# Kernel optimization log

Hardware: AMD Instinct MI355X
Metric: run time of the kernel (lower is better)

## Reference

```python
import jax, jax.numpy as jnp
from jax import lax
import numpy as np

KERNEL_SIZE = 29
N_T = 1000
SIGMA_MIN, SIGMA_MAX = 0.5, 20.0
HIDDEN = 32


def _gaussian_kernel1d(sigma, ksize):
    # torchvision: linspace over [-half, half], normalized gaussian pdf
    half = (ksize - 1) * 0.5
    xg = jnp.linspace(-half, half, ksize)
    pdf = jnp.exp(-0.5 * (xg / sigma) ** 2)
    return pdf / pdf.sum()


def batch_blur(x, sigmas, ksize=KERNEL_SIZE):
    # x: [B,C,H,W], sigmas: [B]. Per-sample separable gaussian blur as a single
    # grouped depthwise conv (feature_group_count = B*C) instead of a Python loop.
    B, C, H, W = x.shape
    k1 = jax.vmap(lambda s: _gaussian_kernel1d(s, ksize))(sigmas)  # [B, k]
    pad = ksize // 2
    xp = jnp.pad(x, ((0, 0), (0, 0), (pad, pad), (pad, pad)), mode='reflect')
    lhs = xp.reshape(1, B * C, H + 2 * pad, W + 2 * pad)
    kbc = jnp.repeat(k1, C, axis=0)  # [B*C, k] per-channel kernel
    # vertical pass then horizontal pass (outer-product 2D kernel == two 1D passes)
    y = lax.conv_general_dilated(lhs, kbc[:, None, :, None], (1, 1), 'VALID',
                                 feature_group_count=B * C)
    y = lax.conv_general_dilated(y, kbc[:, None, None, :], (1, 1), 'VALID',
                                 feature_group_count=B * C)
    return y.reshape(B, C, H, W)


def gt_net(z, tn, W1, b1, tw, W2, b2):
    # simple time-conditioned conv net standing in for the opaque `gt` module
    h = lax.conv_general_dilated(z, W1, (1, 1), 'SAME')  # [B,HIDDEN,H,W]
    h = h + b1[None, :, None, None] + (tn[:, None] * tw[None, :])[:, :, None, None]
    h = jax.nn.relu(h)
    out = lax.conv_general_dilated(h, W2, (1, 1), 'SAME') + b2[None, :, None, None]
    return out


def setup_inputs() -> dict:
    key = jax.random.key(0)
    ks = jax.random.split(key, 6)
    B, C, H, W = 32, 3, 256, 256
    x = jax.random.normal(ks[0], (B, C, H, W), dtype=jnp.float32)
    t = jax.random.randint(ks[1], (B,), 0, N_T, dtype=jnp.int32)
    W1 = jax.random.normal(ks[2], (HIDDEN, C, 3, 3), dtype=jnp.float32) * 0.1
    b1 = jnp.zeros((HIDDEN,), dtype=jnp.float32)
    tw = jax.random.normal(ks[3], (HIDDEN,), dtype=jnp.float32) * 0.1
    W2 = jax.random.normal(ks[4], (C, HIDDEN, 3, 3), dtype=jnp.float32) * 0.1
    b2 = jnp.zeros((C,), dtype=jnp.float32)
    sigma_schedule = jnp.linspace(SIGMA_MIN, SIGMA_MAX, N_T, dtype=jnp.float32)
    return {"x": x, "t": t, "W1": W1, "b1": b1, "tw": tw, "W2": W2, "b2": b2,
            "sigma_schedule": sigma_schedule}


def reference(x, t, W1, b1, tw, W2, b2, sigma_schedule):
    sigma_t = sigma_schedule[t]                      # [B]
    z_t = batch_blur(x, sigma_t, KERNEL_SIZE)        # [B,C,H,W]
    preds = gt_net(z_t, t.astype(jnp.float32) / N_T, W1, b1, tw, W2, b2)
    return jnp.mean((x - preds) ** 2)                # MSELoss
```

## Files before the change

kernel.cpp:

```cpp
#include <hip/hip_runtime.h>
#include <hip/hip_bf16.h>

#define BATCH 32
#define CH 3
#define HH 256
#define WW 256
#define KS 29
#define PAD 14
#define NT_F 1000.0f

typedef __attribute__((ext_vector_type(8))) short short8;
typedef __attribute__((ext_vector_type(4))) float f32x4;
typedef __attribute__((ext_vector_type(16))) float f32x16;

union U4 { short8 s8; uint4 u4; };

__device__ inline unsigned short bf16rne(float f) {
  unsigned u = __float_as_uint(f);
  unsigned r = (u + 0x7FFFu + ((u >> 16) & 1u)) >> 16;
  return (unsigned short)r;
}
__device__ inline unsigned pk_bf16(float a, float b) {
  union { __hip_bfloat162 h2; unsigned u; } cv;
  cv.h2 = __float22bfloat162_rn(make_float2(a, b));
  return cv.u;
}


#define PARTIAL_OFF 3151872

__global__ __launch_bounds__(256, 3) void blur_kernel(
    const float* __restrict__ x, const int* __restrict__ t,
    const float* __restrict__ sched, const float* __restrict__ W1,
    const float* __restrict__ b1, const float* __restrict__ tw,
    const float* __restrict__ W2, float* __restrict__ ws,
    unsigned short* __restrict__ z) {
  int blk = blockIdx.x;
  int tid = threadIdx.x;

  if (blk >= BATCH * CH * 8) {
    float* tcond = ws + 1024;
    unsigned short* w1n = (unsigned short*)(ws + 2048);
    unsigned short* w2c = (unsigned short*)(ws + 2816);
    for (int i = tid; i < 1536; i += 256) {
      int mf = i >> 9, r = i & 511;
      int och = r >> 4, s = r & 15;
      int tp = mf * 4 + (s >> 2), ci = s & 3;
      w1n[i] = (ci < 3 && tp < 9) ? bf16rne(W1[och * 27 + ci * 9 + tp])
                                  : (unsigned short)0;
    }
    for (int i = tid; i < 4608; i += 256) {
      int tap = i >> 9, r = i & 511;
      int n = r >> 5, s = r & 31;
      int och = (s & 3) + 8 * ((s >> 2) & 3) + 4 * (s >> 4);
      int dy = tap / 3, dx = tap - dy * 3;
      w2c[i] = (n < 3) ? bf16rne(W2[((n * 32 + och) * 3 + dy) * 3 + dx])
                       : (unsigned short)0;
    }
    for (int i = tid; i < 1024; i += 256) {
      int b = i >> 5, o = i & 31;
      tcond[i] = b1[o] + ((float)t[b] * (1.0f / NT_F)) * tw[o];
    }
    return;
  }

  {
    int wid = (blk & 7) * 96 + (blk >> 3);
    blk = wid;
  }

  __shared__ float vsp[32][288];
  __shared__ float gkl[32];
  int rg = blk & 7;
  int bc = blk >> 3;
  int b = bc / CH;
  int y0 = rg * 32;
  const float* xp = x + (size_t)bc * (HH * WW);

  float xv[60];
#pragma unroll
  for (int i = 0; i < 60; i++) {
    int gy = y0 - PAD + i;
    gy = (gy < 0) ? -gy : gy;
    gy = (gy >= HH) ? (2 * HH - 2 - gy) : gy;
    xv[i] = xp[gy * WW + tid];
  }

  if (tid < 64) {
    float wexp = 0.0f;
    if (tid < KS) {
      float sigma = sched[t[b]];
      float xg = (float)(tid - PAD) / sigma;
      wexp = expf(-0.5f * xg * xg);
    }
    float s = wexp;
#pragma unroll
    for (int off = 32; off > 0; off >>= 1) s += __shfl_down(s, off);
    float tot = __shfl(s, 0);
    if (tid < 32) gkl[tid] = wexp / tot;
  }
  __syncthreads();

  float acc[32];
#pragma unroll
  for (int yy = 0; yy < 32; yy++) acc[yy] = 0.0f;
#pragma unroll
  for (int kk = 0; kk < KS; kk++) {
    float kv = gkl[kk];
#pragma unroll
    for (int yy = 0; yy < 32; yy++) acc[yy] += kv * xv[yy + kk];
  }
#pragma unroll
  for (int yy = 0; yy < 32; yy++) vsp[yy][tid + 16] = acc[yy];
  __syncthreads();
  {
    int row = tid >> 4, i2 = tid & 15;
#pragma unroll
    for (int r2 = 0; r2 < 2; r2++) {
      int rr = row + 16 * r2;
      vsp[rr][i2] = vsp[rr][32 - i2];
      vsp[rr][272 + i2] = vsp[rr][270 - i2];
    }
  }
  __syncthreads();

  size_t zb = (size_t)bc * (HH * WW);
#pragma unroll
  for (int it = 0; it < 8; ++it) {
    int unit = tid + 256 * it;
    int row = unit >> 6, cg = unit & 63;
    float w[36];
#pragma unroll
    for (int i = 0; i < 9; i++)
      *(float4*)&w[4 * i] = *(const float4*)&vsp[row][4 * (cg + i)];
    float o0 = 0, o1 = 0, o2 = 0, o3 = 0;
#pragma unroll
    for (int kk = 0; kk < KS; kk++) {
      float kv = gkl[kk];
      o0 += kv * w[2 + kk];
      o1 += kv * w[3 + kk];
      o2 += kv * w[4 + kk];
      o3 += kv * w[5 + kk];
    }
    unsigned u0 = pk_bf16(o0, o1);
    unsigned u1 = pk_bf16(o2, o3);
    *(uint2*)&z[zb + (size_t)(y0 + row) * WW + 4 * cg] = make_uint2(u0, u1);
  }
}

__global__ __launch_bounds__(256, 5) void convloss_kernel(
    const float* __restrict__ x, const float* __restrict__ ws,
    const float* __restrict__ b2g, float* __restrict__ partial) {
  __shared__ __align__(16) unsigned short zs4[400 * 4];
  __shared__ __align__(16) unsigned short hs[324 * 40];
  __shared__ float wsum[4];

  const float* tcond = ws + 1024;
  const unsigned short* w1n = (const unsigned short*)(ws + 2048);
  const unsigned short* w2c = (const unsigned short*)(ws + 2816);
  const unsigned short* zg = (const unsigned short*)(ws + 5120);

  int flat = (blockIdx.z * 16 + blockIdx.y) * 16 + blockIdx.x;
  int wid = (flat & 7) * 1024 + (flat >> 3);
  int b = wid >> 8;
  int by = (wid >> 4) & 15;
  int bx = wid & 15;

  int tid = threadIdx.x;
  int x0 = bx * 16, y0 = by * 16;
  const unsigned short* zbp = zg + (size_t)b * 3 * HH * WW;

  int lane = tid & 63;
  int q = lane >> 4;
  int col = lane & 15;
  int col32 = lane & 31;
  int h = lane >> 5;
  int wv = tid >> 6;

  if (tid < 200) {
    int zy = tid / 10;
    int zx2 = tid - zy * 10;
    int gy = y0 - 2 + zy;
    int gx0 = x0 - 2 + 2 * zx2;
    bool ok = ((unsigned)gy < (unsigned)HH) && ((unsigned)gx0 < (unsigned)(WW - 1));
    int cy = (gy < 0) ? 0 : ((gy > 255) ? 255 : gy);
    int cx = (gx0 < 0) ? 0 : ((gx0 > 254) ? 254 : gx0);
    int gi = cy * WW + cx;
    unsigned c0 = *(const unsigned*)&zbp[gi];
    unsigned c1 = *(const unsigned*)&zbp[HH * WW + gi];
    unsigned c2 = *(const unsigned*)&zbp[2 * HH * WW + gi];
    unsigned m = ok ? 0xFFFFFFFFu : 0u;
    c0 &= m; c1 &= m; c2 &= m;
    uint4 o;
    o.x = (c0 & 0xFFFFu) | (c1 << 16);
    o.y = c2 & 0xFFFFu;
    o.z = (c0 >> 16) | (c1 & 0xFFFF0000u);
    o.w = c2 >> 16;
    *(uint4*)&zs4[(zy * 20 + 2 * zx2) * 4] = o;
  }

  U4 W0, W1f, W2f;
  W0.u4  = *(const uint4*)(w1n + 0 * 512 + col32 * 16 + h * 8);
  W1f.u4 = *(const uint4*)(w1n + 1 * 512 + col32 * 16 + h * 8);
  W2f.u4 = *(const uint4*)(w1n + 2 * 512 + col32 * 16 + h * 8);

  f32x16 tc16;
#pragma unroll
  for (int r1 = 0; r1 < 4; r1++) {
    float4 v = *(const float4*)(tcond + b * 32 + 4 * h + 8 * r1);
    tc16[4 * r1 + 0] = v.x;
    tc16[4 * r1 + 1] = v.y;
    tc16[4 * r1 + 2] = v.z;
    tc16[4 * r1 + 3] = v.w;
  }

  int colc = (col < 3) ? col : 0;
  float b2v = b2g[colc];

  const float* xb = x + (size_t)b * 3 * HH * WW;
  float4 xpre[4];
#pragma unroll
  for (int i = 0; i < 4; i++) {
    int g2 = wv * 4 + i;
    xpre[i] = *(const float4*)&xb[colc * (HH * WW) + (y0 + g2) * WW + x0 + q * 4];
  }

  __syncthreads();

  int oA0 = h ? 8 : 0, oB0 = h ? 80 : 4;
  int oA1 = h ? 160 : 84, oB1 = h ? 164 : 88;
  const int oA2 = 168;

#pragma unroll
  for (int i = 0; i < 3; i++) {
    int g = wv + 4 * i;
    if (g < 11) {
      int p = g * 32 + col32;
      int pc = (p > 323) ? 323 : p;
      int py = pc / 18, px = pc - py * 18;
      int ub = (py * 20 + px) * 4;
      uint2 l0 = *(const uint2*)&zs4[ub + oA0];
      uint2 l1 = *(const uint2*)&zs4[ub + oB0];
      uint2 l2 = *(const uint2*)&zs4[ub + oA1];
      uint2 l3 = *(const uint2*)&zs4[ub + oB1];
      uint2 l4 = *(const uint2*)&zs4[ub + oA2];
      U4 Bz0, Bz1, Bz2;
      Bz0.u4 = make_uint4(l0.x, l0.y, l1.x, l1.y);
      Bz1.u4 = make_uint4(l2.x, l2.y, l3.x, l3.y);
      Bz2.u4 = make_uint4(l4.x, l4.y, 0u, 0u);
      f32x16 a = __builtin_amdgcn_mfma_f32_32x32x16_bf16(W0.s8, Bz0.s8, tc16, 0, 0, 0);
      a = __builtin_amdgcn_mfma_f32_32x32x16_bf16(W1f.s8, Bz1.s8, a, 0, 0, 0);
      a = __builtin_amdgcn_mfma_f32_32x32x16_bf16(W2f.s8, Bz2.s8, a, 0, 0, 0);
      if (p < 324) {
        unsigned wpk[8];
#pragma unroll
        for (int m = 0; m < 8; m++)
          wpk[m] = pk_bf16(fmaxf(a[2 * m], 0.0f), fmaxf(a[2 * m + 1], 0.0f));
        *(uint4*)&hs[p * 40 + 16 * h]     = make_uint4(wpk[0], wpk[1], wpk[2], wpk[3]);
        *(uint4*)&hs[p * 40 + 16 * h + 8] = make_uint4(wpk[4], wpk[5], wpk[6], wpk[7]);
      }
    }
  }
  __syncthreads();

  U4 Bt[3][3];
  {
    const unsigned short* wbase = w2c + col * 32 + q * 8;
#pragma unroll
    for (int dy = 0; dy < 3; dy++)
#pragma unroll
      for (int dx = 0; dx < 3; dx++)
        Bt[dy][dx].u4 = *(const uint4*)(wbase + (dy * 3 + dx) * 512);
  }

  const f32x4 bcv = {b2v, b2v, b2v, b2v};
  f32x4 dacc[4];
#pragma unroll
  for (int i = 0; i < 4; i++) dacc[i] = bcv;
  {
    const unsigned short* hbase = &hs[((wv * 4) * 18 + col) * 40 + q * 8];
#pragma unroll
    for (int dx = 0; dx < 3; dx++) {
#pragma unroll
      for (int rr = 0; rr < 6; rr++) {
        U4 A;
        A.u4 = *(const uint4*)&hbase[(rr * 18 + dx) * 40];
        if (rr < 4)
          dacc[rr] = __builtin_amdgcn_mfma_f32_16x16x32_bf16(A.s8, Bt[0][dx].s8, dacc[rr], 0, 0, 0);
        if (rr >= 1 && rr < 5)
          dacc[rr - 1] = __builtin_amdgcn_mfma_f32_16x16x32_bf16(A.s8, Bt[1][dx].s8, dacc[rr - 1], 0, 0, 0);
        if (rr >= 2)
          dacc[rr - 2] = __builtin_amdgcn_mfma_f32_16x16x32_bf16(A.s8, Bt[2][dx].s8, dacc[rr - 2], 0, 0, 0);
      }
    }
  }

  float s = 0.0f;
  if (col < 3) {
#pragma unroll
    for (int i = 0; i < 4; i++) {
      float4 xv = xpre[i];
      float d0 = xv.x - dacc[i][0];
      float d1 = xv.y - dacc[i][1];
      float d2 = xv.z - dacc[i][2];
      float d3 = xv.w - dacc[i][3];
      s += d0 * d0 + d1 * d1 + d2 * d2 + d3 * d3;
    }
  }
#pragma unroll
  for (int off = 32; off > 0; off >>= 1) s += __shfl_down(s, off);
  if (lane == 0) wsum[wv] = s;
  __syncthreads();
  if (tid == 0) {
    int bid = (b * 16 + by) * 16 + bx;
    partial[bid] = wsum[0] + wsum[1] + wsum[2] + wsum[3];
  }
}

__global__ __launch_bounds__(256) void reduce_kernel(const float* __restrict__ partial,
                                                     float* __restrict__ out) {
  __shared__ float wsum[4];
  int tid = threadIdx.x;
  float s = 0.0f;
#pragma unroll
  for (int i = 0; i < 8; i++) {
    float4 v = *(const float4*)&partial[(tid + 256 * i) * 4];
    s += v.x + v.y + v.z + v.w;
  }
#pragma unroll
  for (int off = 32; off > 0; off >>= 1) s += __shfl_down(s, off);
  if ((tid & 63) == 0) wsum[tid >> 6] = s;
  __syncthreads();
  if (tid == 0)
    out[0] = (wsum[0] + wsum[1] + wsum[2] + wsum[3]) * (1.0f / 6291456.0f);
}

extern "C" void kernel_launch(void* const* d_in, const int* in_sizes, int n_in,
                              void* d_out, int out_size, void* d_ws, size_t ws_size,
                              hipStream_t stream) {
  const float* x = (const float*)d_in[0];
  const int* t = (const int*)d_in[1];
  const float* W1 = (const float*)d_in[2];
  const float* b1 = (const float*)d_in[3];
  const float* tw = (const float*)d_in[4];
  const float* W2 = (const float*)d_in[5];
  const float* b2 = (const float*)d_in[6];
  const float* sched = (const float*)d_in[7];
  float* out = (float*)d_out;
  float* ws = (float*)d_ws;
  unsigned short* z = (unsigned short*)(ws + 5120);
  float* partial = ws + PARTIAL_OFF;

  blur_kernel<<<BATCH * CH * 8 + 1, 256, 0, stream>>>(x, t, sched, W1, b1, tw, W2, ws, z);
  dim3 grid(16, 16, BATCH);
  convloss_kernel<<<grid, 256, 0, stream>>>(x, ws, b2, partial);
  reduce_kernel<<<1, 256, 0, stream>>>(partial, out);
}
```

Before: 134.5 us.

## Give each wavefront a private hidden-activation tile and drop block barrier

Each wave now computes the first conv for its own 6x18 halo rows into a per-wave LDS buffer, so the block-wide __syncthreads between the two conv stages is removed. The hidden buffer layout changes from a padded 40-short stride to a 64-byte-per-pixel layout with an XOR swizzle to avoid bank conflicts. This recomputes the overlapping halo rows across waves (108 vs 81 pixels per wave), adding MFMA work and LDS footprint in exchange for no cross-wave synchronisation. Correctness relies on intra-wave ordering of LDS writes and reads with no barrier.

```diff
diff --git a/kernel.cpp b/kernel.cpp
--- a/kernel.cpp
+++ b/kernel.cpp
@@ -152,7 +152,7 @@
     const float* __restrict__ x, const float* __restrict__ ws,
     const float* __restrict__ b2g, float* __restrict__ partial) {
   __shared__ __align__(16) unsigned short zs4[400 * 4];
-  __shared__ __align__(16) unsigned short hs[324 * 40];
+  __shared__ __align__(16) unsigned short hsw[4 * 6 * 18 * 32];
   __shared__ float wsum[4];
 
   const float* tcond = ws + 1024;
@@ -231,37 +231,36 @@
   int oA1 = h ? 160 : 84, oB1 = h ? 164 : 88;
   const int oA2 = 168;
 
-#pragma unroll
-  for (int i = 0; i < 3; i++) {
-    int g = wv + 4 * i;
-    if (g < 11) {
-      int p = g * 32 + col32;
-      int pc = (p > 323) ? 323 : p;
-      int py = pc / 18, px = pc - py * 18;
-      int ub = (py * 20 + px) * 4;
-      uint2 l0 = *(const uint2*)&zs4[ub + oA0];
-      uint2 l1 = *(const uint2*)&zs4[ub + oB0];
-      uint2 l2 = *(const uint2*)&zs4[ub + oA1];
-      uint2 l3 = *(const uint2*)&zs4[ub + oB1];
-      uint2 l4 = *(const uint2*)&zs4[ub + oA2];
-      U4 Bz0, Bz1, Bz2;
-      Bz0.u4 = make_uint4(l0.x, l0.y, l1.x, l1.y);
-      Bz1.u4 = make_uint4(l2.x, l2.y, l3.x, l3.y);
-      Bz2.u4 = make_uint4(l4.x, l4.y, 0u, 0u);
-      f32x16 a = __builtin_amdgcn_mfma_f32_32x32x16_bf16(W0.s8, Bz0.s8, tc16, 0, 0, 0);
-      a = __builtin_amdgcn_mfma_f32_32x32x16_bf16(W1f.s8, Bz1.s8, a, 0, 0, 0);
-      a = __builtin_amdgcn_mfma_f32_32x32x16_bf16(W2f.s8, Bz2.s8, a, 0, 0, 0);
-      if (p < 324) {
-        unsigned wpk[8];
-#pragma unroll
-        for (int m = 0; m < 8; m++)
-          wpk[m] = pk_bf16(fmaxf(a[2 * m], 0.0f), fmaxf(a[2 * m + 1], 0.0f));
-        *(uint4*)&hs[p * 40 + 16 * h]     = make_uint4(wpk[0], wpk[1], wpk[2], wpk[3]);
-        *(uint4*)&hs[p * 40 + 16 * h + 8] = make_uint4(wpk[4], wpk[5], wpk[6], wpk[7]);
-      }
-    }
-  }
-  __syncthreads();
+  char* hbw = (char*)hsw + wv * 6912;
+#pragma unroll
+  for (int g2 = 0; g2 < 4; g2++) {
+    int e = g2 * 32 + col32;
+    int ec = (e > 107) ? 107 : e;
+    int row_l = ec / 18;
+    int px = ec - row_l * 18;
+    int ub = ((4 * wv + row_l) * 20 + px) * 4;
+    uint2 l0 = *(const uint2*)&zs4[ub + oA0];
+    uint2 l1 = *(const uint2*)&zs4[ub + oB0];
+    uint2 l2 = *(const uint2*)&zs4[ub + oA1];
+    uint2 l3 = *(const uint2*)&zs4[ub + oB1];
+    uint2 l4 = *(const uint2*)&zs4[ub + oA2];
+    U4 Bz0, Bz1, Bz2;
+    Bz0.u4 = make_uint4(l0.x, l0.y, l1.x, l1.y);
+    Bz1.u4 = make_uint4(l2.x, l2.y, l3.x, l3.y);
+    Bz2.u4 = make_uint4(l4.x, l4.y, 0u, 0u);
+    f32x16 a = __builtin_amdgcn_mfma_f32_32x32x16_bf16(W0.s8, Bz0.s8, tc16, 0, 0, 0);
+    a = __builtin_amdgcn_mfma_f32_32x32x16_bf16(W1f.s8, Bz1.s8, a, 0, 0, 0);
+    a = __builtin_amdgcn_mfma_f32_32x32x16_bf16(W2f.s8, Bz2.s8, a, 0, 0, 0);
+    if (e < 108) {
+      unsigned wpk[8];
+#pragma unroll
+      for (int m = 0; m < 8; m++)
+        wpk[m] = pk_bf16(fmaxf(a[2 * m], 0.0f), fmaxf(a[2 * m + 1], 0.0f));
+      int wb = row_l * 1152 + px * 64 + ((32 * h) ^ ((px & 2) << 4));
+      *(uint4*)(hbw + wb)      = make_uint4(wpk[0], wpk[1], wpk[2], wpk[3]);
+      *(uint4*)(hbw + wb + 16) = make_uint4(wpk[4], wpk[5], wpk[6], wpk[7]);
+    }
+  }
 
   U4 Bt[3][3];
   {
@@ -278,13 +277,15 @@
 #pragma unroll
   for (int i = 0; i < 4; i++) dacc[i] = bcv;
   {
-    const unsigned short* hbase = &hs[((wv * 4) * 18 + col) * 40 + q * 8];
+    const char* hb = (const char*)hsw + wv * 6912;
 #pragma unroll
     for (int dx = 0; dx < 3; dx++) {
+      int px = col + dx;
+      const char* bp = hb + px * 64 + ((q * 16) ^ ((px & 2) << 4));
 #pragma unroll
       for (int rr = 0; rr < 6; rr++) {
         U4 A;
-        A.u4 = *(const uint4*)&hbase[(rr * 18 + dx) * 40];
+        A.u4 = *(const uint4*)(bp + rr * 1152);
         if (rr < 4)
           dacc[rr] = __builtin_amdgcn_mfma_f32_16x16x32_bf16(A.s8, Bt[0][dx].s8, dacc[rr], 0, 0, 0);
         if (rr >= 1 && rr < 5)
```

Result: no change. 137.0 us (+1.8%).
